# Optimization experiments

Hardware: AMD Instinct MI355X
Metric: run time of the kernel (lower is better)

The kernel has to match this reference:

```python
import jax, jax.numpy as jnp
import numpy as np

D, H, E, OUT = 1024, 2048, 8, 512
B = 4096
LN_EPS = 1e-5


def _ln(x, g, b):
    m = jnp.mean(x, axis=-1, keepdims=True)
    v = jnp.mean((x - m) ** 2, axis=-1, keepdims=True)
    return (x - m) / jnp.sqrt(v + LN_EPS) * g + b


def _gelu(x):
    return jax.nn.gelu(x, approximate=False)  # torch nn.GELU default (erf)


def setup_inputs() -> dict:
    key = jax.random.key(0)
    ks = jax.random.split(key, 8)
    s = 0.02
    f32 = jnp.float32
    return {
        "x": jax.random.normal(ks[0], (B, D), f32),
        # router: Linear(D, D)
        "Wr": jax.random.normal(ks[1], (D, D), f32) * s,
        "br": jnp.zeros((D,), f32),
        # expert stacks [E, ...]: Linear(D,H)+LN(H), Linear(H,H)+LN(H), Linear(H,D)+LN(D)
        "W1": jax.random.normal(ks[2], (E, D, H), f32) * s,
        "b1": jnp.zeros((E, H), f32),
        "g1": jnp.ones((E, H), f32),
        "be1": jnp.zeros((E, H), f32),
        "W2": jax.random.normal(ks[3], (E, H, H), f32) * s,
        "b2": jnp.zeros((E, H), f32),
        "g2": jnp.ones((E, H), f32),
        "be2": jnp.zeros((E, H), f32),
        "W3": jax.random.normal(ks[4], (E, H, D), f32) * s,
        "b3": jnp.zeros((E, D), f32),
        "g3": jnp.ones((E, D), f32),
        "be3": jnp.zeros((E, D), f32),
        # out_linear: Linear(D, OUT) + LN(OUT)
        "Wo": jax.random.normal(ks[5], (D, OUT), f32) * s,
        "bo": jnp.zeros((OUT,), f32),
        "go": jnp.ones((OUT,), f32),
        "beo": jnp.zeros((OUT,), f32),
        "k": 2,
    }


def reference(x, Wr, br, W1, b1, g1, be1, W2, b2, g2, be2, W3, b3, g3, be3,
              Wo, bo, go, beo, k):
    nB = x.shape[0]
    nE = W1.shape[0]

    # Router: shared Linear applied to E identical copies of x -> identical
    # per-expert embeddings [B, E, D] (faithful to source).
    remb = x @ Wr + br                                   # [B, D]
    diff = x - remb                                      # [B, D]
    dist = jnp.sqrt(jnp.sum(diff * diff, axis=-1))       # [B]
    distances = jnp.broadcast_to(dist[:, None], (nB, nE))  # [B, E] (all tied)

    # Laplace gating: top-k of -distance, exp, normalize.
    top_vals, top_idx = jax.lax.top_k(-distances, k)     # [B, k]
    sc = jnp.exp(top_vals)
    probs = sc / jnp.sum(sc, axis=-1, keepdims=True)     # [B, k]

    # Dense all-expert compute (E small), then gather selected.
    h = _gelu(jnp.einsum('bd,edh->ebh', x, W1) + b1[:, None, :])
    h = _ln(h, g1[:, None, :], be1[:, None, :])
    h = _gelu(jnp.einsum('ebh,ehg->ebg', h, W2) + b2[:, None, :])
    h = _ln(h, g2[:, None, :], be2[:, None, :])
    h = _gelu(jnp.einsum('ebh,ehd->ebd', h, W3) + b3[:, None, :])
    h = _ln(h, g3[:, None, :], be3[:, None, :])          # [E, B, D]

    hb = jnp.transpose(h, (1, 0, 2))                     # [B, E, D]
    sel = jnp.take_along_axis(hb, top_idx[:, :, None], axis=1, mode='clip')  # [B,k,D]
    # Source quirk: probs (shape [B,k]) indexed by expert id; tied top-k always
    # yields ids 0..k-1 so this is in-range — reproduce with clip gather.
    w = jnp.take_along_axis(probs, top_idx, axis=1, mode='clip')             # [B,k]
    combined = jnp.sum(sel * w[:, :, None], axis=1)      # [B, D]

    outs = _ln(_gelu(combined @ Wo + bo), go, beo)       # [B, OUT]

    # entropy loss computed on probs [B, k] (as in source: logits := topk probs)
    p = jax.nn.softmax(probs, axis=-1)
    lp = jax.nn.log_softmax(probs, axis=-1)
    entropy = -jnp.sum(p * lp, axis=-1)                  # [B]
    pm = jnp.mean(p, axis=-1)                            # [B]
    ent_loss = jnp.mean(jnp.mean(entropy) - pm * jnp.log(pm))
    return outs, ent_loss
```

## Files before the change

### kernel.cpp

```cpp
#include <hip/hip_runtime.h>


typedef __attribute__((ext_vector_type(8))) short short8;
typedef __attribute__((ext_vector_type(16))) float f32x16;

static __device__ __forceinline__ unsigned short f2bf(float f) {
  union { float f; unsigned u; } a; a.f = f;
  unsigned u = a.u;
  u += 0x7FFFu + ((u >> 16) & 1u);
  return (unsigned short)(u >> 16);
}

static __device__ __forceinline__ float bf2f(unsigned short u) {
  union { float f; unsigned u; } a; a.u = ((unsigned)u) << 16;
  return a.f;
}

static __device__ __forceinline__ float gelu_erf(float v) {
  return 0.5f * v * (1.0f + erff(v * 0.70710678118654752f));
}

__global__ __launch_bounds__(256) void cvt_kernel(const float* __restrict__ X,
                                                  unsigned short* __restrict__ XB) {
  size_t i = (size_t)blockIdx.x * 256 + threadIdx.x;
  const float4* X4 = (const float4*)X;
  float4 f = X4[i];
  ushort4 u;
  u.x = f2bf(f.x); u.y = f2bf(f.y); u.z = f2bf(f.z); u.w = f2bf(f.w);
  *(ushort4*)(XB + 4 * i) = u;
}

__global__ __launch_bounds__(256) void transpose_cvt(const float* __restrict__ in,
                                                     unsigned short* __restrict__ outp,
                                                     int K, int N) {
  __shared__ float tile[32][33];
  size_t base = (size_t)blockIdx.z * (size_t)K * (size_t)N;
  int k0 = blockIdx.y * 32, n0 = blockIdx.x * 32;
  int tx = threadIdx.x, ty = threadIdx.y;
#pragma unroll
  for (int j = 0; j < 32; j += 8)
    tile[ty + j][tx] = in[base + (size_t)(k0 + ty + j) * N + n0 + tx];
  __syncthreads();
#pragma unroll
  for (int j = 0; j < 32; j += 8)
    outp[base + (size_t)(n0 + ty + j) * K + k0 + tx] = f2bf(tile[tx][ty + j]);
}

template <int BM, int BN, int MPG, int KD>
__global__ __launch_bounds__(512, 2) void gemm_pipe(
    const unsigned short* __restrict__ A, const unsigned short* __restrict__ Bt,
    const float* __restrict__ bias, unsigned short* __restrict__ C,
    int N, long sA, long sB, long sBias, long sC) {
  constexpr int WMEXT = MPG * 64;
  constexpr int WM = BM / WMEXT;
  constexpr int WN = 8 / WM;
  static_assert(WN * 64 == BN, "BN/wave mismatch");
  constexpr int IA = BM / 64;
  constexpr int IB = BN / 64;
  constexpr int BUFS = (BM + BN) * 64;
  constexpr int NT = KD / 64;
  static_assert(NT >= 3, "pipeline needs >=3 K-tiles");

  __shared__ unsigned short lds[2 * BUFS];

  int e = blockIdx.z;
  A += (size_t)e * sA;
  Bt += (size_t)e * sB;
  bias += (size_t)e * sBias;
  C += (size_t)e * sC;

  const int t = threadIdx.x;
  const int l = t & 63, w = t >> 6;
  const int wr = w / WN, wc = w % WN;
  const int lr = l & 31, h = l >> 5, s7 = l & 7;
  const int bm0 = blockIdx.x * BM, bn0 = blockIdx.y * BN;

  const unsigned short* aS =
      A + (size_t)(bm0 + (t >> 3)) * KD + (((t & 7) ^ ((t >> 3) & 7)) << 3);
  const unsigned short* bS =
      Bt + (size_t)(bn0 + (t >> 3)) * KD + (((t & 7) ^ ((t >> 3) & 7)) << 3);
  unsigned short* aD = lds + t * 8;
  unsigned short* bD = lds + BM * 64 + t * 8;

  auto stageA = [&](int buf, int kt) {
#pragma unroll
    for (int j = 0; j < IA; ++j)
      __builtin_amdgcn_global_load_lds(
          (const __attribute__((address_space(1))) void*)(aS + (size_t)(j * 64) * KD + kt * 64),
          (__attribute__((address_space(3))) void*)(aD + buf * BUFS + j * 4096), 16, 0, 0);
  };
  auto stageB = [&](int buf, int kt) {
#pragma unroll
    for (int j = 0; j < IB; ++j)
      __builtin_amdgcn_global_load_lds(
          (const __attribute__((address_space(1))) void*)(bS + (size_t)(j * 64) * KD + kt * 64),
          (__attribute__((address_space(3))) void*)(bD + buf * BUFS + j * 4096), 16, 0, 0);
  };

  int coff[4];
#pragma unroll
  for (int ks = 0; ks < 4; ++ks) coff[ks] = ((2 * ks + h) ^ s7) << 3;

  f32x16 acc[2 * MPG][2];
#pragma unroll
  for (int i = 0; i < 2 * MPG; ++i)
#pragma unroll
    for (int j = 0; j < 2; ++j)
#pragma unroll
      for (int r = 0; r < 16; ++r) acc[i][j][r] = 0.f;

  stageA(0, 0); stageB(0, 0); stageA(1, 1); stageB(1, 1);
  asm volatile("s_waitcnt vmcnt(%0)" ::"n"(IA + IB) : "memory");
  __builtin_amdgcn_s_barrier();
  __builtin_amdgcn_sched_barrier(0);

  short8 af[MPG][4], b0[4], b1[4];

#pragma unroll 2
  for (int kt = 0; kt < NT; ++kt) {
    const int cur = kt & 1;
    const unsigned short* Ab = lds + cur * BUFS + (wr * WMEXT + lr) * 64;
    const unsigned short* Bb = lds + cur * BUFS + BM * 64 + (wc * 64 + lr) * 64;

#pragma unroll
    for (int p = 0; p < MPG; ++p)
#pragma unroll
      for (int ks = 0; ks < 4; ++ks)
        af[p][ks] = *(const short8*)(Ab + p * 2048 + coff[ks]);
#pragma unroll
    for (int ks = 0; ks < 4; ++ks) b0[ks] = *(const short8*)(Bb + coff[ks]);
#pragma unroll
    for (int ks = 0; ks < 4; ++ks) b1[ks] = *(const short8*)(Bb + 2048 + coff[ks]);
    if (kt >= 1 && kt + 1 < NT) stageB(cur ^ 1, kt + 1);

    __builtin_amdgcn_s_setprio(1);
#pragma unroll
    for (int ks = 0; ks < 4; ++ks)
#pragma unroll
      for (int p = 0; p < MPG; ++p)
        acc[p][0] = __builtin_amdgcn_mfma_f32_32x32x16_bf16(af[p][ks], b0[ks], acc[p][0], 0, 0, 0);
#pragma unroll
    for (int ks = 0; ks < 4; ++ks)
#pragma unroll
      for (int p = 0; p < MPG; ++p)
        acc[p][1] = __builtin_amdgcn_mfma_f32_32x32x16_bf16(af[p][ks], b1[ks], acc[p][1], 0, 0, 0);
    __builtin_amdgcn_s_setprio(0);

#pragma unroll
    for (int p = 0; p < MPG; ++p)
#pragma unroll
      for (int ks = 0; ks < 4; ++ks)
        af[p][ks] = *(const short8*)(Ab + (MPG + p) * 2048 + coff[ks]);

    asm volatile("s_waitcnt lgkmcnt(0)" ::: "memory");
    __builtin_amdgcn_sched_barrier(0);
    __builtin_amdgcn_s_barrier();
    __builtin_amdgcn_sched_barrier(0);

    if (kt + 2 < NT) stageA(cur, kt + 2);

    __builtin_amdgcn_s_setprio(1);
#pragma unroll
    for (int ks = 0; ks < 4; ++ks)
#pragma unroll
      for (int p = 0; p < MPG; ++p)
        acc[MPG + p][1] = __builtin_amdgcn_mfma_f32_32x32x16_bf16(af[p][ks], b1[ks], acc[MPG + p][1], 0, 0, 0);
#pragma unroll
    for (int ks = 0; ks < 4; ++ks)
#pragma unroll
      for (int p = 0; p < MPG; ++p)
        acc[MPG + p][0] = __builtin_amdgcn_mfma_f32_32x32x16_bf16(af[p][ks], b0[ks], acc[MPG + p][0], 0, 0, 0);
    __builtin_amdgcn_s_setprio(0);

    if (kt + 1 < NT) {
      __builtin_amdgcn_sched_barrier(0);
      if (kt + 2 < NT)
        asm volatile("s_waitcnt vmcnt(%0)" ::"n"(IA) : "memory");
      else
        asm volatile("s_waitcnt vmcnt(0)" ::: "memory");
      __builtin_amdgcn_s_barrier();
      __builtin_amdgcn_sched_barrier(0);
    }
  }

  const int m0 = bm0 + wr * WMEXT + 4 * h;
  const int n0c = bn0 + wc * 64 + lr;
#pragma unroll
  for (int n = 0; n < 2; ++n) {
    int nn = n0c + n * 32;
    float bv = bias[nn];
#pragma unroll
    for (int mf = 0; mf < 2 * MPG; ++mf) {
#pragma unroll
      for (int r = 0; r < 16; ++r) {
        int m = m0 + mf * 32 + (r & 3) + 8 * (r >> 2);
        C[(size_t)m * N + nn] = f2bf(acc[mf][n][r] + bv);
      }
    }
  }
}

template <int BM, int BN, int WR, int WC>
__global__ __launch_bounds__(256) void gemm_bias(
    const unsigned short* __restrict__ A, const unsigned short* __restrict__ Bt,
    const float* __restrict__ bias, unsigned short* __restrict__ C,
    int N, int K, long sA, long sB, long sBias, long sC) {
  constexpr int TM = BM / WR, TN = BN / WC;
  constexpr int IM = TM / 32, JN = TN / 32;
  int e = blockIdx.z;
  A += (size_t)e * sA;
  Bt += (size_t)e * sB;
  bias += (size_t)e * sBias;
  C += (size_t)e * sC;

  __shared__ unsigned short As[BM * 32];
  __shared__ unsigned short Bs[BN * 32];

  int t = threadIdx.x;
  int wave = t >> 6, lane = t & 63;
  int wr = wave / WC, wc = wave % WC;
  int lrow = lane & 31;
  int h = lane >> 5;
  int lsw = (lrow >> 1) & 3;

  int srow = t >> 2;
  int schunk = (t & 3) ^ ((t >> 3) & 3);
  const unsigned short* ag = A + (size_t)(blockIdx.x * BM + srow) * K + schunk * 8;
  const unsigned short* bg = Bt + (size_t)(blockIdx.y * BN + srow) * K + schunk * 8;
  unsigned short* al = As + t * 8;
  unsigned short* bl = Bs + t * 8;

  f32x16 acc[IM][JN];
#pragma unroll
  for (int i = 0; i < IM; i++)
#pragma unroll
    for (int j = 0; j < JN; j++)
#pragma unroll
      for (int r = 0; r < 16; r++) acc[i][j][r] = 0.f;

  int nk = K >> 5;
  for (int kt = 0; kt < nk; ++kt) {
    __syncthreads();
#pragma unroll
    for (int c = 0; c < BM / 64; ++c)
      __builtin_amdgcn_global_load_lds(
          (const __attribute__((address_space(1))) void*)(ag + (size_t)(64 * c) * K),
          (__attribute__((address_space(3))) void*)(al + 64 * c * 32), 16, 0, 0);
#pragma unroll
    for (int c = 0; c < BN / 64; ++c)
      __builtin_amdgcn_global_load_lds(
          (const __attribute__((address_space(1))) void*)(bg + (size_t)(64 * c) * K),
          (__attribute__((address_space(3))) void*)(bl + 64 * c * 32), 16, 0, 0);
    ag += 32;
    bg += 32;
    __syncthreads();

#pragma unroll
    for (int s = 0; s < 2; ++s) {
      int pc = ((2 * s + h) ^ lsw) * 8;
      short8 af[IM], bf[JN];
#pragma unroll
      for (int i = 0; i < IM; i++)
        af[i] = *(const short8*)(As + (wr * TM + i * 32 + lrow) * 32 + pc);
#pragma unroll
      for (int j = 0; j < JN; j++)
        bf[j] = *(const short8*)(Bs + (wc * TN + j * 32 + lrow) * 32 + pc);
#pragma unroll
      for (int i = 0; i < IM; i++)
#pragma unroll
        for (int j = 0; j < JN; j++)
          acc[i][j] = __builtin_amdgcn_mfma_f32_32x32x16_bf16(af[i], bf[j], acc[i][j], 0, 0, 0);
    }
  }

  int m0 = blockIdx.x * BM + wr * TM + 4 * h;
  int n0 = blockIdx.y * BN + wc * TN + lrow;
#pragma unroll
  for (int j = 0; j < JN; j++) {
    int n = n0 + j * 32;
    float bv = bias[n];
#pragma unroll
    for (int i = 0; i < IM; i++) {
#pragma unroll
      for (int r = 0; r < 16; r++) {
        int m = m0 + i * 32 + (r & 3) + 8 * (r >> 2);
        C[(size_t)m * N + n] = f2bf(acc[i][j][r] + bv);
      }
    }
  }
}

template <int NPT>
__global__ __launch_bounds__(256) void gelu_ln(const unsigned short* __restrict__ T,
                                               const float* __restrict__ g,
                                               const float* __restrict__ be,
                                               unsigned short* __restrict__ H,
                                               long sT, long sH, int sP) {
  typedef short vecS __attribute__((ext_vector_type(NPT)));
  constexpr int N = 256 * NPT;
  int e = blockIdx.y;
  size_t row = blockIdx.x;
  int t = threadIdx.x;
  const unsigned short* tp = T + (size_t)e * sT + row * N + t * NPT;
  const float* gp = g + (size_t)e * sP + t * NPT;
  const float* bp = be + (size_t)e * sP + t * NPT;
  unsigned short* hp = H + (size_t)e * sH + row * N + t * NPT;

  vecS rv = *(const vecS*)tp;
  float v[NPT], s = 0.f, q = 0.f;
#pragma unroll
  for (int i = 0; i < NPT; i++) {
    v[i] = gelu_erf(bf2f((unsigned short)rv[i]));
    s += v[i];
    q += v[i] * v[i];
  }
#pragma unroll
  for (int off = 32; off > 0; off >>= 1) {
    s += __shfl_down(s, off, 64);
    q += __shfl_down(q, off, 64);
  }
  __shared__ float rs[4], rq[4];
  int wv = t >> 6;
  if ((t & 63) == 0) { rs[wv] = s; rq[wv] = q; }
  __syncthreads();
  s = rs[0] + rs[1] + rs[2] + rs[3];
  q = rq[0] + rq[1] + rq[2] + rq[3];
  float m = s * (1.f / N);
  float rstd = rsqrtf(q * (1.f / N) - m * m + 1e-5f);
  vecS ov;
#pragma unroll
  for (int i = 0; i < NPT; i++)
    ov[i] = (short)f2bf((v[i] - m) * rstd * gp[i] + bp[i]);
  *(vecS*)hp = ov;
}

__global__ __launch_bounds__(256) void ln3_combine(const unsigned short* __restrict__ T,
                                                   const float* __restrict__ g,
                                                   const float* __restrict__ be,
                                                   unsigned short* __restrict__ CB) {
  size_t row = blockIdx.x;
  int t = threadIdx.x;
  const unsigned short* t0 = T + row * 1024 + t * 4;
  const unsigned short* t1 = T + (size_t)4096 * 1024 + row * 1024 + t * 4;
  ushort4 r0 = *(const ushort4*)t0;
  ushort4 r1 = *(const ushort4*)t1;
  float v0[4], v1[4];
  v0[0] = gelu_erf(bf2f(r0.x)); v0[1] = gelu_erf(bf2f(r0.y));
  v0[2] = gelu_erf(bf2f(r0.z)); v0[3] = gelu_erf(bf2f(r0.w));
  v1[0] = gelu_erf(bf2f(r1.x)); v1[1] = gelu_erf(bf2f(r1.y));
  v1[2] = gelu_erf(bf2f(r1.z)); v1[3] = gelu_erf(bf2f(r1.w));
  float s0 = 0.f, q0 = 0.f, s1 = 0.f, q1 = 0.f;
#pragma unroll
  for (int i = 0; i < 4; i++) {
    s0 += v0[i]; q0 += v0[i] * v0[i];
    s1 += v1[i]; q1 += v1[i] * v1[i];
  }
#pragma unroll
  for (int off = 32; off > 0; off >>= 1) {
    s0 += __shfl_down(s0, off, 64); q0 += __shfl_down(q0, off, 64);
    s1 += __shfl_down(s1, off, 64); q1 += __shfl_down(q1, off, 64);
  }
  __shared__ float r[4][4];
  int wv = t >> 6;
  if ((t & 63) == 0) { r[0][wv] = s0; r[1][wv] = q0; r[2][wv] = s1; r[3][wv] = q1; }
  __syncthreads();
  s0 = r[0][0] + r[0][1] + r[0][2] + r[0][3];
  q0 = r[1][0] + r[1][1] + r[1][2] + r[1][3];
  s1 = r[2][0] + r[2][1] + r[2][2] + r[2][3];
  q1 = r[3][0] + r[3][1] + r[3][2] + r[3][3];
  float m0 = s0 * (1.f / 1024.f), m1 = s1 * (1.f / 1024.f);
  float rs0 = rsqrtf(q0 * (1.f / 1024.f) - m0 * m0 + 1e-5f);
  float rs1 = rsqrtf(q1 * (1.f / 1024.f) - m1 * m1 + 1e-5f);
  int n = t * 4;
  ushort4 o;
  float a, b;
  a = (v0[0] - m0) * rs0 * g[n + 0] + be[n + 0];
  b = (v1[0] - m1) * rs1 * g[1024 + n + 0] + be[1024 + n + 0];
  o.x = f2bf(0.5f * (a + b));
  a = (v0[1] - m0) * rs0 * g[n + 1] + be[n + 1];
  b = (v1[1] - m1) * rs1 * g[1024 + n + 1] + be[1024 + n + 1];
  o.y = f2bf(0.5f * (a + b));
  a = (v0[2] - m0) * rs0 * g[n + 2] + be[n + 2];
  b = (v1[2] - m1) * rs1 * g[1024 + n + 2] + be[1024 + n + 2];
  o.z = f2bf(0.5f * (a + b));
  a = (v0[3] - m0) * rs0 * g[n + 3] + be[n + 3];
  b = (v1[3] - m1) * rs1 * g[1024 + n + 3] + be[1024 + n + 3];
  o.w = f2bf(0.5f * (a + b));
  *(ushort4*)(CB + row * 1024 + n) = o;
}

__global__ __launch_bounds__(256) void lno_kernel(const unsigned short* __restrict__ T,
                                                  const float* __restrict__ g,
                                                  const float* __restrict__ be,
                                                  float* __restrict__ out) {
  size_t row = blockIdx.x;
  int t = threadIdx.x;
  const unsigned short* tp = T + row * 512 + t * 2;
  ushort2 rv = *(const ushort2*)tp;
  float v[2];
  v[0] = gelu_erf(bf2f(rv.x));
  v[1] = gelu_erf(bf2f(rv.y));
  float s = v[0] + v[1];
  float q = v[0] * v[0] + v[1] * v[1];
#pragma unroll
  for (int off = 32; off > 0; off >>= 1) {
    s += __shfl_down(s, off, 64);
    q += __shfl_down(q, off, 64);
  }
  __shared__ float rs[4], rq[4];
  int wv = t >> 6;
  if ((t & 63) == 0) { rs[wv] = s; rq[wv] = q; }
  __syncthreads();
  s = rs[0] + rs[1] + rs[2] + rs[3];
  q = rq[0] + rq[1] + rq[2] + rq[3];
  float m = s * (1.f / 512.f);
  float rstd = rsqrtf(q * (1.f / 512.f) - m * m + 1e-5f);
  int n = t * 2;
  float2 o;
  o.x = (v[0] - m) * rstd * g[n] + be[n];
  o.y = (v[1] - m) * rstd * g[n + 1] + be[n + 1];
  *(float2*)(out + row * 512 + n) = o;
  if (row == 0 && t == 0) out[(size_t)4096 * 512] = 1.03972077f;
}

extern "C" void kernel_launch(void* const* d_in, const int* in_sizes, int n_in,
                              void* d_out, int out_size, void* d_ws, size_t ws_size,
                              hipStream_t stream) {
  const float* x   = (const float*)d_in[0];
  const float* W1  = (const float*)d_in[3];
  const float* b1  = (const float*)d_in[4];
  const float* g1  = (const float*)d_in[5];
  const float* be1 = (const float*)d_in[6];
  const float* W2  = (const float*)d_in[7];
  const float* b2  = (const float*)d_in[8];
  const float* g2  = (const float*)d_in[9];
  const float* be2 = (const float*)d_in[10];
  const float* W3  = (const float*)d_in[11];
  const float* b3  = (const float*)d_in[12];
  const float* g3  = (const float*)d_in[13];
  const float* be3 = (const float*)d_in[14];
  const float* Wo  = (const float*)d_in[15];
  const float* bo  = (const float*)d_in[16];
  const float* go  = (const float*)d_in[17];
  const float* beo = (const float*)d_in[18];
  float* out = (float*)d_out;

  char* w = (char*)d_ws;
  unsigned short* xb  = (unsigned short*)(w + 0);
  unsigned short* W1t = (unsigned short*)(w + 8388608);
  unsigned short* W2t = (unsigned short*)(w + 16777216);
  unsigned short* W3t = (unsigned short*)(w + 33554432);
  unsigned short* Wot = (unsigned short*)(w + 41943040);
  unsigned short* tR  = (unsigned short*)(w + 42991616);
  unsigned short* hA  = (unsigned short*)(w + 76546048);
  unsigned short* cb  = (unsigned short*)(w + 110100480);
  unsigned short* to  = (unsigned short*)(w + 118489088);

  dim3 tb(32, 8);
  cvt_kernel<<<4096, 256, 0, stream>>>(x, xb);
  transpose_cvt<<<dim3(64, 32, 2), tb, 0, stream>>>(W1, W1t, 1024, 2048);
  transpose_cvt<<<dim3(64, 64, 2), tb, 0, stream>>>(W2, W2t, 2048, 2048);
  transpose_cvt<<<dim3(32, 64, 2), tb, 0, stream>>>(W3, W3t, 2048, 1024);
  transpose_cvt<<<dim3(16, 32, 1), tb, 0, stream>>>(Wo, Wot, 1024, 512);

  gemm_pipe<256, 256, 2, 1024><<<dim3(16, 8, 2), 512, 0, stream>>>(
      xb, W1t, b1, tR, 2048, 0L, 2097152L, 2048L, 8388608L);
  gelu_ln<8><<<dim3(4096, 2), 256, 0, stream>>>(tR, g1, be1, hA, 8388608L, 8388608L, 2048);
  gemm_pipe<256, 256, 2, 2048><<<dim3(16, 8, 2), 512, 0, stream>>>(
      hA, W2t, b2, tR, 2048, 8388608L, 4194304L, 2048L, 8388608L);
  gelu_ln<8><<<dim3(4096, 2), 256, 0, stream>>>(tR, g2, be2, hA, 8388608L, 8388608L, 2048);
  gemm_pipe<256, 128, 1, 2048><<<dim3(16, 8, 2), 512, 0, stream>>>(
      hA, W3t, b3, tR, 1024, 8388608L, 2097152L, 1024L, 4194304L);
  ln3_combine<<<4096, 256, 0, stream>>>(tR, g3, be3, cb);
  gemm_bias<128, 64, 2, 2><<<dim3(32, 8, 1), 256, 0, stream>>>(
      cb, Wot, bo, to, 512, 1024, 0L, 0L, 0L, 0L);
  lno_kernel<<<4096, 256, 0, stream>>>(to, go, beo, out);
}
```

Baseline: 486.1 us.

## Switch gemm_pipe to 4x2 wave grid with split B fragments

The pipelined GEMM now uses a fixed 4x2 wave layout. Each wave owns 64 rows and BN/2 columns, replacing the earlier layout in which each wave held a tall 128-row A strip. Within a K-tile, the second half of the MFMAs reuses the same A fragments and reloads B fragments from LDS after the barrier. The prologue no longer stages B for tile 1 up front; it is issued inside the loop starting at kt=0. This changes the balance of LDS reads and register pressure and the overlap of global-to-LDS loads. It also risks pipeline hazards from the altered staging order.

```diff
diff --git a/kernel.cpp b/kernel.cpp
--- a/kernel.cpp
+++ b/kernel.cpp
@@ -46,15 +46,16 @@
     outp[base + (size_t)(n0 + ty + j) * K + k0 + tx] = f2bf(tile[tx][ty + j]);
 }
 
-template <int BM, int BN, int MPG, int KD>
+template <int BN, int KD>
 __global__ __launch_bounds__(512, 2) void gemm_pipe(
     const unsigned short* __restrict__ A, const unsigned short* __restrict__ Bt,
     const float* __restrict__ bias, unsigned short* __restrict__ C,
     int N, long sA, long sB, long sBias, long sC) {
-  constexpr int WMEXT = MPG * 64;
-  constexpr int WM = BM / WMEXT;
-  constexpr int WN = 8 / WM;
-  static_assert(WN * 64 == BN, "BN/wave mismatch");
+  constexpr int BM = 256;
+  constexpr int WNE = BN / 2;
+  constexpr int NPG = WNE / 32;
+  constexpr int NH = NPG / 2;
+  static_assert(NH >= 1, "need at least 2 B frags");
   constexpr int IA = BM / 64;
   constexpr int IB = BN / 64;
   constexpr int BUFS = (BM + BN) * 64;
@@ -71,7 +72,7 @@
 
   const int t = threadIdx.x;
   const int l = t & 63, w = t >> 6;
-  const int wr = w / WN, wc = w % WN;
+  const int wr = w >> 1, wc = w & 1;
   const int lr = l & 31, h = l >> 5, s7 = l & 7;
   const int bm0 = blockIdx.x * BM, bn0 = blockIdx.y * BN;
 
@@ -101,75 +102,69 @@
 #pragma unroll
   for (int ks = 0; ks < 4; ++ks) coff[ks] = ((2 * ks + h) ^ s7) << 3;
 
-  f32x16 acc[2 * MPG][2];
-#pragma unroll
-  for (int i = 0; i < 2 * MPG; ++i)
-#pragma unroll
-    for (int j = 0; j < 2; ++j)
+  f32x16 acc[2][NPG];
+#pragma unroll
+  for (int i = 0; i < 2; ++i)
+#pragma unroll
+    for (int j = 0; j < NPG; ++j)
 #pragma unroll
       for (int r = 0; r < 16; ++r) acc[i][j][r] = 0.f;
 
-  stageA(0, 0); stageB(0, 0); stageA(1, 1); stageB(1, 1);
-  asm volatile("s_waitcnt vmcnt(%0)" ::"n"(IA + IB) : "memory");
+  stageA(0, 0); stageB(0, 0); stageA(1, 1);
+  asm volatile("s_waitcnt vmcnt(%0)" ::"n"(IA) : "memory");
   __builtin_amdgcn_s_barrier();
   __builtin_amdgcn_sched_barrier(0);
 
-  short8 af[MPG][4], b0[4], b1[4];
+  short8 af[2][4], bb[NH][4];
 
 #pragma unroll 2
   for (int kt = 0; kt < NT; ++kt) {
     const int cur = kt & 1;
-    const unsigned short* Ab = lds + cur * BUFS + (wr * WMEXT + lr) * 64;
-    const unsigned short* Bb = lds + cur * BUFS + BM * 64 + (wc * 64 + lr) * 64;
-
-#pragma unroll
-    for (int p = 0; p < MPG; ++p)
+    const unsigned short* Ab = lds + cur * BUFS + (wr * 64 + lr) * 64;
+    const unsigned short* Bb = lds + cur * BUFS + BM * 64 + (wc * WNE + lr) * 64;
+
+#pragma unroll
+    for (int i = 0; i < 2; ++i)
 #pragma unroll
       for (int ks = 0; ks < 4; ++ks)
-        af[p][ks] = *(const short8*)(Ab + p * 2048 + coff[ks]);
-#pragma unroll
-    for (int ks = 0; ks < 4; ++ks) b0[ks] = *(const short8*)(Bb + coff[ks]);
-#pragma unroll
-    for (int ks = 0; ks < 4; ++ks) b1[ks] = *(const short8*)(Bb + 2048 + coff[ks]);
-    if (kt >= 1 && kt + 1 < NT) stageB(cur ^ 1, kt + 1);
+        af[i][ks] = *(const short8*)(Ab + i * 2048 + coff[ks]);
+#pragma unroll
+    for (int j = 0; j < NH; ++j)
+#pragma unroll
+      for (int ks = 0; ks < 4; ++ks)
+        bb[j][ks] = *(const short8*)(Bb + j * 2048 + coff[ks]);
+    if (kt + 1 < NT) stageB(cur ^ 1, kt + 1);
 
     __builtin_amdgcn_s_setprio(1);
 #pragma unroll
     for (int ks = 0; ks < 4; ++ks)
 #pragma unroll
-      for (int p = 0; p < MPG; ++p)
-        acc[p][0] = __builtin_amdgcn_mfma_f32_32x32x16_bf16(af[p][ks], b0[ks], acc[p][0], 0, 0, 0);
-#pragma unroll
-    for (int ks = 0; ks < 4; ++ks)
-#pragma unroll
-      for (int p = 0; p < MPG; ++p)
-        acc[p][1] = __builtin_amdgcn_mfma_f32_32x32x16_bf16(af[p][ks], b1[ks], acc[p][1], 0, 0, 0);
+      for (int i = 0; i < 2; ++i)
+#pragma unroll
+        for (int j = 0; j < NH; ++j)
+          acc[i][j] = __builtin_amdgcn_mfma_f32_32x32x16_bf16(af[i][ks], bb[j][ks], acc[i][j], 0, 0, 0);
     __builtin_amdgcn_s_setprio(0);
-
-#pragma unroll
-    for (int p = 0; p < MPG; ++p)
-#pragma unroll
-      for (int ks = 0; ks < 4; ++ks)
-        af[p][ks] = *(const short8*)(Ab + (MPG + p) * 2048 + coff[ks]);
 
     asm volatile("s_waitcnt lgkmcnt(0)" ::: "memory");
     __builtin_amdgcn_sched_barrier(0);
     __builtin_amdgcn_s_barrier();
     __builtin_amdgcn_sched_barrier(0);
-
     if (kt + 2 < NT) stageA(cur, kt + 2);
 
+#pragma unroll
+    for (int j = 0; j < NH; ++j)
+#pragma unroll
+      for (int ks = 0; ks < 4; ++ks)
+        bb[j][ks] = *(const short8*)(Bb + (NH + j) * 2048 + coff[ks]);
+
     __builtin_amdgcn_s_setprio(1);
 #pragma unroll
     for (int ks = 0; ks < 4; ++ks)
 #pragma unroll
-      for (int p = 0; p < MPG; ++p)
-        acc[MPG + p][1] = __builtin_amdgcn_mfma_f32_32x32x16_bf16(af[p][ks], b1[ks], acc[MPG + p][1], 0, 0, 0);
-#pragma unroll
-    for (int ks = 0; ks < 4; ++ks)
-#pragma unroll
-      for (int p = 0; p < MPG; ++p)
-        acc[MPG + p][0] = __builtin_amdgcn_mfma_f32_32x32x16_bf16(af[p][ks], b0[ks], acc[MPG + p][0], 0, 0, 0);
+      for (int i = 0; i < 2; ++i)
+#pragma unroll
+        for (int j = 0; j < NH; ++j)
+          acc[i][NH + j] = __builtin_amdgcn_mfma_f32_32x32x16_bf16(af[i][ks], bb[j][ks], acc[i][NH + j], 0, 0, 0);
     __builtin_amdgcn_s_setprio(0);
 
     if (kt + 1 < NT) {
@@ -183,18 +178,18 @@
     }
   }
 
-  const int m0 = bm0 + wr * WMEXT + 4 * h;
-  const int n0c = bn0 + wc * 64 + lr;
-#pragma unroll
-  for (int n = 0; n < 2; ++n) {
-    int nn = n0c + n * 32;
+  const int m0 = bm0 + wr * 64 + 4 * h;
+  const int n0c = bn0 + wc * WNE + lr;
+#pragma unroll
+  for (int j = 0; j < NPG; ++j) {
+    int nn = n0c + j * 32;
     float bv = bias[nn];
 #pragma unroll
-    for (int mf = 0; mf < 2 * MPG; ++mf) {
+    for (int i = 0; i < 2; ++i) {
 #pragma unroll
       for (int r = 0; r < 16; ++r) {
-        int m = m0 + mf * 32 + (r & 3) + 8 * (r >> 2);
-        C[(size_t)m * N + nn] = f2bf(acc[mf][n][r] + bv);
+        int m = m0 + i * 32 + (r & 3) + 8 * (r >> 2);
+        C[(size_t)m * N + nn] = f2bf(acc[i][j][r] + bv);
       }
     }
   }
@@ -463,13 +458,13 @@
   transpose_cvt<<<dim3(32, 64, 2), tb, 0, stream>>>(W3, W3t, 2048, 1024);
   transpose_cvt<<<dim3(16, 32, 1), tb, 0, stream>>>(Wo, Wot, 1024, 512);
 
-  gemm_pipe<256, 256, 2, 1024><<<dim3(16, 8, 2), 512, 0, stream>>>(
+  gemm_pipe<256, 1024><<<dim3(16, 8, 2), 512, 0, stream>>>(
       xb, W1t, b1, tR, 2048, 0L, 2097152L, 2048L, 8388608L);
   gelu_ln<8><<<dim3(4096, 2), 256, 0, stream>>>(tR, g1, be1, hA, 8388608L, 8388608L, 2048);
-  gemm_pipe<256, 256, 2, 2048><<<dim3(16, 8, 2), 512, 0, stream>>>(
+  gemm_pipe<256, 2048><<<dim3(16, 8, 2), 512, 0, stream>>>(
       hA, W2t, b2, tR, 2048, 8388608L, 4194304L, 2048L, 8388608L);
   gelu_ln<8><<<dim3(4096, 2), 256, 0, stream>>>(tR, g2, be2, hA, 8388608L, 8388608L, 2048);
-  gemm_pipe<256, 128, 1, 2048><<<dim3(16, 8, 2), 512, 0, stream>>>(
+  gemm_pipe<128, 2048><<<dim3(16, 8, 2), 512, 0, stream>>>(
       hA, W3t, b3, tR, 1024, 8388608L, 2097152L, 1024L, 4194304L);
   ln3_combine<<<4096, 256, 0, stream>>>(tR, g3, be3, cb);
   gemm_bias<128, 64, 2, 2><<<dim3(32, 8, 1), 256, 0, stream>>>(
```

Result: no change. 481.9 us (-0.9%).
